# Performance work log

Measured on AMD Instinct MI355X. Metric: run time of the kernel, lower is better.

## Reference

```python
import jax, jax.numpy as jnp
import numpy as np

B, S, HID = 1, 2048, 2880
H, KV, D = 64, 8, 64
WINDOW = 128
SCALE = D ** -0.5
NEG_INF = jnp.float32(-1e30)


def _rope_cos_sin():
    # realistic RoPE tables over full head_dim (HF rotate_half convention)
    inv_freq = 1.0 / (10000.0 ** (np.arange(0, D, 2, dtype=np.float32) / D))
    t = np.arange(S, dtype=np.float32)
    freqs = np.outer(t, inv_freq)                      # [S, D/2]
    emb = np.concatenate([freqs, freqs], axis=-1)      # [S, D]
    return jnp.asarray(np.cos(emb))[None], jnp.asarray(np.sin(emb))[None]


def setup_inputs() -> dict:
    key = jax.random.key(0)
    ks = jax.random.split(key, 10)
    cos, sin = _rope_cos_sin()
    sd = lambda fan_in: 1.0 / np.sqrt(fan_in)
    return {
        "hidden_states": jax.random.normal(ks[0], (B, S, HID), jnp.float32),
        "cos": cos, "sin": sin,
        "Wq": jax.random.normal(ks[1], (HID, H * D), jnp.float32) * sd(HID),
        "bq": jax.random.normal(ks[2], (H * D,), jnp.float32) * 0.02,
        "Wk": jax.random.normal(ks[3], (HID, KV * D), jnp.float32) * sd(HID),
        "bk": jax.random.normal(ks[4], (KV * D,), jnp.float32) * 0.02,
        "Wv": jax.random.normal(ks[5], (HID, KV * D), jnp.float32) * sd(HID),
        "bv": jax.random.normal(ks[6], (KV * D,), jnp.float32) * 0.02,
        "Wo": jax.random.normal(ks[7], (H * D, HID), jnp.float32) * sd(H * D),
        "bo": jax.random.normal(ks[8], (HID,), jnp.float32) * 0.02,
        "sinks": jax.random.normal(ks[9], (H,), jnp.float32),
    }


def _rotate_half(x):
    x1, x2 = jnp.split(x, 2, axis=-1)
    return jnp.concatenate([-x2, x1], axis=-1)


def _forward(hidden_states, cos, sin, Wq, bq, Wk, bk, Wv, bv, Wo, bo, sinks):
    q = (hidden_states @ Wq + bq).reshape(B, S, H, D)
    k = (hidden_states @ Wk + bk).reshape(B, S, KV, D)
    v = (hidden_states @ Wv + bv).reshape(B, S, KV, D)
    # RoPE with explicit cos/sin, unsqueeze at head dim (bsnd layout)
    c, s = cos[:, :, None, :], sin[:, :, None, :]
    q = q * c + _rotate_half(q) * s
    k = k * c + _rotate_half(k) * s
    # GQA: expand kv heads to match query heads
    k = jnp.repeat(k, H // KV, axis=2)
    v = jnp.repeat(v, H // KV, axis=2)
    scores = jnp.einsum("bqhd,bkhd->bhqk", q, k) * SCALE  # [B,H,S,S]
    i = jnp.arange(S)[:, None]
    j = jnp.arange(S)[None, :]
    allowed = (j <= i) & (j > i - WINDOW)                  # causal + sliding window
    scores = jnp.where(allowed, scores, NEG_INF)
    # sink-augmented softmax: sinks act as an extra logit per head, dropped after norm
    m = jnp.maximum(scores.max(axis=-1), sinks[None, :, None])  # [B,H,S]
    p = jnp.exp(scores - m[..., None])                      # [B,H,S,S]
    denom = p.sum(axis=-1) + jnp.exp(sinks[None, :, None] - m)  # [B,H,S]
    attn = jnp.einsum("bhqk,bkhd->bqhd", p, v) / denom.transpose(0, 2, 1)[..., None]
    return attn.reshape(B, S, H * D) @ Wo + bo


def reference(hidden_states, cos, sin, Wq, bq, Wk, bk, Wv, bv, Wo, bo, sinks):
    return _forward(hidden_states, cos, sin, Wq, bq, Wk, bk, Wv, bv, Wo, bo, sinks)
```

## Files before the change

kernel.cpp:

```cpp
#include <hip/hip_runtime.h>

typedef unsigned short u16;
typedef __bf16 bf16x8 __attribute__((ext_vector_type(8)));
typedef float f32x4 __attribute__((ext_vector_type(4)));

constexpr int SEQ = 2048;
constexpr int HIDN = 2880;
constexpr int NQKV = 5120;
constexpr float SCALE = 0.125f;
constexpr float NEG_INF = -1e30f;

#define ASM_VMCNT(n)  asm volatile("s_waitcnt vmcnt(" #n ")" ::: "memory")
#define ASM_LGKM(n)   asm volatile("s_waitcnt lgkmcnt(" #n ")" ::: "memory")
#define ASM_BARRIER() asm volatile("s_barrier" ::: "memory")
#define SCHEDBAR()    __builtin_amdgcn_sched_barrier(0)

__device__ __forceinline__ u16 f2bf(float f) {
  unsigned int u = __builtin_bit_cast(unsigned int, f);
  u += 0x7FFFu + ((u >> 16) & 1u);
  return (u16)(u >> 16);
}
__device__ __forceinline__ float bf2f(u16 h) {
  unsigned int u = ((unsigned int)h) << 16;
  return __builtin_bit_cast(float, u);
}
__device__ __forceinline__ void async_load16(const void* g, void* l) {
  __builtin_amdgcn_global_load_lds(
      (const __attribute__((address_space(1))) unsigned int*)g,
      (__attribute__((address_space(3))) unsigned int*)l, 16, 0, 0);
}
__device__ __forceinline__ f32x4 DSR(unsigned addr) {
  f32x4 d;
  asm volatile("ds_read_b128 %0, %1" : "=v"(d) : "v"(addr));
  return d;
}
__device__ __forceinline__ bf16x8 asbf(f32x4 v) { return __builtin_bit_cast(bf16x8, v); }

__global__ __launch_bounds__(256) void conv_f2b(const float* __restrict__ in,
                                                u16* __restrict__ out, long n4) {
  long i = (long)blockIdx.x * 256 + threadIdx.x;
  if (i >= n4) return;
  float4 v = ((const float4*)in)[i];
  u16 o0 = f2bf(v.x), o1 = f2bf(v.y), o2 = f2bf(v.z), o3 = f2bf(v.w);
  out[i * 4 + 0] = o0; out[i * 4 + 1] = o1; out[i * 4 + 2] = o2; out[i * 4 + 3] = o3;
}

__global__ __launch_bounds__(256) void transpose_f2b(const float* __restrict__ in,
                                                     u16* __restrict__ out,
                                                     int R, int C, int ostride) {
  __shared__ float tile[32][33];
  int c0 = blockIdx.x * 32, r0 = blockIdx.y * 32;
  int tx = threadIdx.x & 31, ty = threadIdx.x >> 5;
#pragma unroll
  for (int i = 0; i < 32; i += 8)
    tile[ty + i][tx] = in[(long)(r0 + ty + i) * C + c0 + tx];
  __syncthreads();
#pragma unroll
  for (int i = 0; i < 32; i += 8)
    out[(long)(c0 + ty + i) * ostride + r0 + tx] = f2bf(tile[tx][ty + i]);
}

__global__ __launch_bounds__(256) void concat_bias(const float* bq, const float* bk,
                                                   const float* bv, float* out) {
  int t = blockIdx.x * 256 + threadIdx.x;
  if (t < 4096) out[t] = bq[t];
  else if (t < 4608) out[t] = bk[t - 4096];
  else if (t < 5120) out[t] = bv[t - 4608];
}

template <int MODE>
__global__ __launch_bounds__(256, 2) void gemm_p2(const u16* __restrict__ A,
                                                  const u16* __restrict__ Bp,
                                                  const float* __restrict__ bias,
                                                  const float* __restrict__ cosb,
                                                  const float* __restrict__ sinb,
                                                  void* __restrict__ out0,
                                                  float* __restrict__ out1,
                                                  int N, int Kst, int nkt) {
  __shared__ u16 lds[28672];
  const int tid = threadIdx.x, lane = tid & 63, wid = tid >> 6;
  const int lr = lane & 15, lk = lane >> 4;

  const int gm = gridDim.x;
  int nwg = gm * gridDim.y;
  int bid = blockIdx.y * gm + blockIdx.x;
  int q8 = nwg >> 3, r8 = nwg & 7;
  int xcd = bid & 7, seq = bid >> 3;
  int swz = (xcd < r8 ? xcd * (q8 + 1) : r8 * (q8 + 1) + (xcd - r8) * q8) + seq;
  const long brow = (long)(swz % gm) * 128;
  const long bcol = (long)(swz / gm) * 256;
  const long kbase = (MODE == 1) ? (long)blockIdx.z * nkt * 32 : 0;

  char* L = (char*)lds;
  const u16* Asrc[2];
  const u16* Bsrc[4];
#pragma unroll
  for (int i = 0; i < 2; ++i) {
    int c = tid + 256 * i;
    Asrc[i] = A + (brow + (c >> 2)) * (long)Kst + kbase + ((c & 3) ^ ((c >> 3) & 3)) * 8;
  }
#pragma unroll
  for (int i = 0; i < 4; ++i) {
    int c = tid + 256 * i;
    Bsrc[i] = Bp + (bcol + (c >> 2)) * (long)Kst + kbase + ((c & 3) ^ ((c >> 3) & 3)) * 8;
  }
  auto stageA = [&](int kt, int ab) {
    char* d = L + ab * 8192;
    async_load16(Asrc[0] + (long)kt * 32, d + tid * 16);
    async_load16(Asrc[1] + (long)kt * 32, d + (tid + 256) * 16);
  };
  auto stageB = [&](int kt) {
    char* d = L + 24576 + (kt & 1) * 16384;
#pragma unroll
    for (int i = 0; i < 4; ++i)
      async_load16(Bsrc[i] + (long)kt * 32, d + (tid + 256 * i) * 16);
  };

  const unsigned lds0 = (unsigned)(size_t)L;
  const unsigned xs = (unsigned)((lk ^ ((lr >> 1) & 3)) << 4);
  const unsigned aoff = lds0 + (unsigned)(lr * 64) + xs;
  const unsigned boff = lds0 + 24576u + (unsigned)((wid * 64 + lr) * 64) + xs;

  f32x4 acc[8][4] = {};
  stageA(0, 0); stageB(0); stageA(1, 1); stageB(1);
  ASM_VMCNT(6);
  ASM_BARRIER();

  int a3 = 0;
  for (int t = 0; t < nkt; ++t) {
    const unsigned ab = aoff + (unsigned)(a3 * 8192);
    const unsigned bb = boff + (unsigned)((t & 1) * 16384);
    const bool s2 = (t + 2 < nkt);
    const int a3n = (a3 == 2) ? 0 : a3 + 1;
    const int a3s = (a3n == 2) ? 0 : a3n + 1;
    f32x4 a[4], b[4];
#pragma unroll
    for (int mf = 0; mf < 4; ++mf) a[mf] = DSR(ab + mf * 1024u);
#pragma unroll
    for (int nf = 0; nf < 4; ++nf) b[nf] = DSR(bb + nf * 1024u);
    if (s2) stageA(t + 2, a3s);
    ASM_BARRIER();
    ASM_LGKM(0); SCHEDBAR();
    __builtin_amdgcn_s_setprio(1);
#pragma unroll
    for (int mf = 0; mf < 4; ++mf)
#pragma unroll
      for (int nf = 0; nf < 4; ++nf)
        acc[mf][nf] = __builtin_amdgcn_mfma_f32_16x16x32_bf16(asbf(a[mf]), asbf(b[nf]), acc[mf][nf], 0, 0, 0);
    __builtin_amdgcn_s_setprio(0);
    ASM_BARRIER();
#pragma unroll
    for (int mf = 0; mf < 4; ++mf) a[mf] = DSR(ab + (mf + 4) * 1024u);
    if (s2) stageB(t + 2);
    ASM_BARRIER();
    ASM_LGKM(0); SCHEDBAR();
    __builtin_amdgcn_s_setprio(1);
#pragma unroll
    for (int mf = 0; mf < 4; ++mf)
#pragma unroll
      for (int nf = 0; nf < 4; ++nf)
        acc[mf + 4][nf] = __builtin_amdgcn_mfma_f32_16x16x32_bf16(asbf(a[mf]), asbf(b[nf]), acc[mf + 4][nf], 0, 0, 0);
    __builtin_amdgcn_s_setprio(0);
    if (s2) { ASM_VMCNT(6); } else { ASM_VMCNT(0); }
    ASM_BARRIER();
    a3 = a3n;
  }

  const int col0 = (int)bcol + wid * 64;
  if (MODE == 0) {
    const bool rope = (col0 < 4608);
#pragma unroll
    for (int mf = 0; mf < 8; ++mf) {
      long row = brow + mf * 16 + lk * 4;
#pragma unroll
      for (int r = 0; r < 4; ++r) {
        long s = row + r;
        if (rope) {
#pragma unroll
          for (int nf = 0; nf < 2; ++nf) {
            int col = col0 + nf * 16 + lr;
            int d = nf * 16 + lr;
            float c = cosb[s * 64 + d], sn = sinb[s * 64 + d];
            float x1 = acc[mf][nf][r] + bias[col];
            float x2 = acc[mf][nf + 2][r] + bias[col + 32];
            ((u16*)out0)[s * (long)N + col]      = f2bf(x1 * c - x2 * sn);
            ((u16*)out0)[s * (long)N + col + 32] = f2bf(x2 * c + x1 * sn);
          }
        } else {
#pragma unroll
          for (int nf = 0; nf < 4; ++nf) {
            int col = col0 + nf * 16 + lr;
            ((u16*)out0)[s * (long)N + col] = f2bf(acc[mf][nf][r] + bias[col]);
          }
        }
      }
    }
  } else {
    float* o = (blockIdx.z == 0) ? (float*)out0 : out1;
#pragma unroll
    for (int mf = 0; mf < 8; ++mf) {
      long row = brow + mf * 16 + lk * 4;
#pragma unroll
      for (int nf = 0; nf < 4; ++nf) {
        int col = col0 + nf * 16 + lr;
        if (col < N) {
#pragma unroll
          for (int r = 0; r < 4; ++r)
            o[(row + r) * (long)N + col] = acc[mf][nf][r];
        }
      }
    }
  }
}

__global__ __launch_bounds__(256) void combine_out(const float* __restrict__ P1,
                                                   const float* __restrict__ bias,
                                                   float* __restrict__ out) {
  long i = (long)blockIdx.x * 256 + threadIdx.x;
  if (i >= (long)SEQ * HIDN / 4) return;
  int c4 = (int)(i % (HIDN / 4));
  float4 p0 = ((const float4*)out)[i];
  float4 p1 = ((const float4*)P1)[i];
  float4 b = ((const float4*)bias)[c4];
  float4 r;
  r.x = p0.x + p1.x + b.x; r.y = p0.y + p1.y + b.y;
  r.z = p0.z + p1.z + b.z; r.w = p0.w + p1.w + b.w;
  ((float4*)out)[i] = r;
}

__global__ __launch_bounds__(256, 1) void attn_kernel(const u16* __restrict__ QKV,
                                                      const float* __restrict__ sinks,
                                                      u16* __restrict__ Oa) {
  __shared__ u16 Ks[64 * 64];
  __shared__ u16 Vt[64 * 64];
  __shared__ u16 Ps[4][64 * 72];
  const int tid = threadIdx.x, wid = tid >> 6, lane = tid & 63;
  const int lr = lane & 15, lk = lane >> 4;
  const int i0 = blockIdx.x * 64;
  const int h = blockIdx.y * 4 + wid;
  const int g = h >> 3;

  bf16x8 qf[4][2];
#pragma unroll
  for (int m = 0; m < 4; ++m)
#pragma unroll
    for (int kc = 0; kc < 2; ++kc)
      qf[m][kc] = *(const bf16x8*)&QKV[(long)(i0 + m * 16 + lr) * NQKV + h * 64 + kc * 32 + lk * 8];

  const float sinkh = sinks[h];
  float mrun[4][4], lrun[4][4];
  f32x4 oacc[4][4] = {};
#pragma unroll
  for (int m = 0; m < 4; ++m)
#pragma unroll
    for (int r = 0; r < 4; ++r) { mrun[m][r] = sinkh; lrun[m][r] = 0.f; }

  const int jb0 = (i0 >= 128) ? (i0 - 128) : 0;
  for (int jb = jb0; jb <= i0; jb += 64) {
#pragma unroll
    for (int i = 0; i < 2; ++i) {
      int c = wid * 128 + i * 64 + lane;
      int row = c >> 3, sp = c & 7;
      int ssrc = sp ^ (row & 7);
      async_load16(QKV + (long)(jb + row) * NQKV + 4096 + g * 64 + ssrc * 8,
                   ((char*)Ks) + c * 16);
    }
    {
      int j0 = (tid & 31) * 2, d0 = (tid >> 5) * 8;
      const u16* vp = QKV + (long)(jb + j0) * NQKV + 4608 + g * 64 + d0;
      int4 rv0 = *(const int4*)vp;
      int4 rv1 = *(const int4*)(vp + NQKV);
      const u16* a0 = (const u16*)&rv0;
      const u16* a1 = (const u16*)&rv1;
#pragma unroll
      for (int e = 0; e < 8; ++e) {
        int d = d0 + e;
        unsigned val = (unsigned)a0[e] | ((unsigned)a1[e] << 16);
        int byt = d * 128 + ((((j0 >> 3) ^ (d & 7)) << 4)) + ((j0 & 7) * 2);
        *(unsigned*)((char*)Vt + byt) = val;
      }
    }
    __syncthreads();

    f32x4 sf[4][4] = {};
    __builtin_amdgcn_s_setprio(1);
#pragma unroll
    for (int kc = 0; kc < 2; ++kc) {
      bf16x8 kf[4];
#pragma unroll
      for (int cf = 0; cf < 4; ++cf) {
        int row = cf * 16 + lr;
        kf[cf] = *(const bf16x8*)((const char*)Ks + row * 128 + (((kc * 4 + lk) ^ (lr & 7)) << 4));
      }
#pragma unroll
      for (int m = 0; m < 4; ++m)
#pragma unroll
        for (int cf = 0; cf < 4; ++cf)
          sf[m][cf] = __builtin_amdgcn_mfma_f32_16x16x32_bf16(qf[m][kc], kf[cf], sf[m][cf], 0, 0, 0);
    }
    __builtin_amdgcn_s_setprio(0);

#pragma unroll
    for (int m = 0; m < 4; ++m) {
      float rmax[4];
#pragma unroll
      for (int r = 0; r < 4; ++r) {
        int i = i0 + m * 16 + lk * 4 + r;
        float mx = NEG_INF;
#pragma unroll
        for (int cf = 0; cf < 4; ++cf) {
          int j = jb + cf * 16 + lr;
          float v = sf[m][cf][r] * SCALE;
          bool ok = (j <= i) && (j > i - 128);
          v = ok ? v : NEG_INF;
          sf[m][cf][r] = v;
          mx = fmaxf(mx, v);
        }
#pragma unroll
        for (int off = 1; off < 16; off <<= 1) mx = fmaxf(mx, __shfl_xor(mx, off, 64));
        rmax[r] = mx;
      }
#pragma unroll
      for (int r = 0; r < 4; ++r) {
        float mnew = fmaxf(mrun[m][r], rmax[r]);
        float corr = __expf(mrun[m][r] - mnew);
        mrun[m][r] = mnew;
        float rsum = 0.f;
#pragma unroll
        for (int cf = 0; cf < 4; ++cf) {
          float p = __expf(sf[m][cf][r] - mnew);
          sf[m][cf][r] = p;
          rsum += p;
        }
#pragma unroll
        for (int off = 1; off < 16; off <<= 1) rsum += __shfl_xor(rsum, off, 64);
        lrun[m][r] = lrun[m][r] * corr + rsum;
#pragma unroll
        for (int dn = 0; dn < 4; ++dn) oacc[m][dn][r] *= corr;
      }
    }

#pragma unroll
    for (int m = 0; m < 4; ++m)
#pragma unroll
      for (int cf = 0; cf < 4; ++cf)
#pragma unroll
        for (int r = 0; r < 4; ++r)
          Ps[wid][(m * 16 + lk * 4 + r) * 72 + cf * 16 + lr] = f2bf(sf[m][cf][r]);
    __syncthreads();

    __builtin_amdgcn_s_setprio(1);
#pragma unroll
    for (int kc = 0; kc < 2; ++kc) {
      bf16x8 pf[4], vf[4];
#pragma unroll
      for (int m = 0; m < 4; ++m)
        pf[m] = *(const bf16x8*)&Ps[wid][(m * 16 + lr) * 72 + kc * 32 + lk * 8];
#pragma unroll
      for (int dn = 0; dn < 4; ++dn) {
        int row = dn * 16 + lr;
        vf[dn] = *(const bf16x8*)((const char*)Vt + row * 128 + (((kc * 4 + lk) ^ (lr & 7)) << 4));
      }
#pragma unroll
      for (int m = 0; m < 4; ++m)
#pragma unroll
        for (int dn = 0; dn < 4; ++dn)
          oacc[m][dn] = __builtin_amdgcn_mfma_f32_16x16x32_bf16(pf[m], vf[dn], oacc[m][dn], 0, 0, 0);
    }
    __builtin_amdgcn_s_setprio(0);
    __syncthreads();
  }

#pragma unroll
  for (int m = 0; m < 4; ++m)
#pragma unroll
    for (int r = 0; r < 4; ++r) {
      float denom = lrun[m][r] + __expf(sinkh - mrun[m][r]);
      float inv = 1.f / denom;
      long row = i0 + m * 16 + lk * 4 + r;
#pragma unroll
      for (int dn = 0; dn < 4; ++dn)
        Oa[row * 4096 + h * 64 + dn * 16 + lr] = f2bf(oacc[m][dn][r] * inv);
    }
}

extern "C" void kernel_launch(void* const* d_in, const int* in_sizes, int n_in,
                              void* d_out, int out_size, void* d_ws, size_t ws_size,
                              hipStream_t stream) {
  const float* X    = (const float*)d_in[0];
  const float* cosb = (const float*)d_in[1];
  const float* sinb = (const float*)d_in[2];
  const float* Wq   = (const float*)d_in[3];
  const float* bq   = (const float*)d_in[4];
  const float* Wk   = (const float*)d_in[5];
  const float* bk   = (const float*)d_in[6];
  const float* Wv   = (const float*)d_in[7];
  const float* bv   = (const float*)d_in[8];
  const float* Wo   = (const float*)d_in[9];
  const float* bo   = (const float*)d_in[10];
  const float* sinks = (const float*)d_in[11];

  char* ws = (char*)d_ws;
  size_t off = 0;
  auto alloc = [&](size_t bytes) -> void* {
    void* p = ws + off;
    off += (bytes + 255) & ~(size_t)255;
    return p;
  };
  u16*   Xb    = (u16*)alloc((size_t)SEQ * HIDN * 2);
  u16*   Wqkv  = (u16*)alloc((size_t)NQKV * HIDN * 2);
  u16*   Wot   = (u16*)alloc((size_t)3072 * 4096 * 2);
  float* bqkv  = (float*)alloc((size_t)NQKV * 4);
  u16*   QKV   = (u16*)alloc((size_t)SEQ * NQKV * 2);
  u16*   Ab    = (u16*)alloc((size_t)SEQ * 4096 * 2);
  float* Pt1 = (float*)Wqkv;
  (void)ws_size; (void)in_sizes; (void)n_in; (void)out_size;

  conv_f2b<<<(SEQ * HIDN / 4 + 255) / 256, 256, 0, stream>>>(X, Xb, (long)SEQ * HIDN / 4);
  transpose_f2b<<<dim3(4096 / 32, HIDN / 32), 256, 0, stream>>>(Wq, Wqkv, HIDN, 4096, HIDN);
  transpose_f2b<<<dim3(512 / 32, HIDN / 32), 256, 0, stream>>>(Wk, Wqkv + (size_t)4096 * HIDN, HIDN, 512, HIDN);
  transpose_f2b<<<dim3(512 / 32, HIDN / 32), 256, 0, stream>>>(Wv, Wqkv + (size_t)4608 * HIDN, HIDN, 512, HIDN);
  transpose_f2b<<<dim3(HIDN / 32, 4096 / 32), 256, 0, stream>>>(Wo, Wot, 4096, HIDN, 4096);
  concat_bias<<<(NQKV + 255) / 256, 256, 0, stream>>>(bq, bk, bv, bqkv);
  gemm_p2<0><<<dim3(16, 20, 1), 256, 0, stream>>>(Xb, Wqkv, bqkv, cosb, sinb,
                                                  QKV, nullptr, NQKV, HIDN, 90);
  attn_kernel<<<dim3(SEQ / 64, 64 / 4), 256, 0, stream>>>(QKV, sinks, Ab);
  gemm_p2<1><<<dim3(16, 12, 2), 256, 0, stream>>>(Ab, Wot, nullptr, nullptr, nullptr,
                                                  d_out, Pt1, HIDN, 4096, 64);
  combine_out<<<(SEQ * HIDN / 4 + 255) / 256, 256, 0, stream>>>(Pt1, bo, (float*)d_out);
}
```

Baseline: 246.8 us.

## Use 8-wave 256x256 GEMM tiles and merge QKV weight transposes into one launch

Result: no change. 246.3 us (-0.2%).

```diff
diff --git a/kernel.cpp b/kernel.cpp
--- a/kernel.cpp
+++ b/kernel.cpp
@@ -45,6 +45,26 @@
   out[i * 4 + 0] = o0; out[i * 4 + 1] = o1; out[i * 4 + 2] = o2; out[i * 4 + 3] = o3;
 }
 
+__global__ __launch_bounds__(256) void transpose_qkv(const float* __restrict__ Wq,
+                                                     const float* __restrict__ Wk,
+                                                     const float* __restrict__ Wv,
+                                                     u16* __restrict__ out) {
+  __shared__ float tile[32][33];
+  int c0 = blockIdx.x * 32, r0 = blockIdx.y * 32;
+  int tx = threadIdx.x & 31, ty = threadIdx.x >> 5;
+  const float* src; int C, cl;
+  if (c0 < 4096)      { src = Wq; C = 4096; cl = c0; }
+  else if (c0 < 4608) { src = Wk; C = 512;  cl = c0 - 4096; }
+  else                { src = Wv; C = 512;  cl = c0 - 4608; }
+#pragma unroll
+  for (int i = 0; i < 32; i += 8)
+    tile[ty + i][tx] = src[(long)(r0 + ty + i) * C + cl + tx];
+  __syncthreads();
+#pragma unroll
+  for (int i = 0; i < 32; i += 8)
+    out[(long)(c0 + ty + i) * HIDN + r0 + tx] = f2bf(tile[tx][ty + i]);
+}
+
 __global__ __launch_bounds__(256) void transpose_f2b(const float* __restrict__ in,
                                                      u16* __restrict__ out,
                                                      int R, int C, int ostride) {
@@ -69,7 +89,7 @@
 }
 
 template <int MODE>
-__global__ __launch_bounds__(256, 2) void gemm_p2(const u16* __restrict__ A,
+__global__ __launch_bounds__(512, 2) void gemm_8w(const u16* __restrict__ A,
                                                   const u16* __restrict__ Bp,
                                                   const float* __restrict__ bias,
                                                   const float* __restrict__ cosb,
@@ -77,8 +97,9 @@
                                                   void* __restrict__ out0,
                                                   float* __restrict__ out1,
                                                   int N, int Kst, int nkt) {
-  __shared__ u16 lds[28672];
+  __shared__ u16 lds[40960];
   const int tid = threadIdx.x, lane = tid & 63, wid = tid >> 6;
+  const int wm = wid >> 2, wn = wid & 3;
   const int lr = lane & 15, lk = lane >> 4;
 
   const int gm = gridDim.x;
@@ -87,48 +108,44 @@
   int q8 = nwg >> 3, r8 = nwg & 7;
   int xcd = bid & 7, seq = bid >> 3;
   int swz = (xcd < r8 ? xcd * (q8 + 1) : r8 * (q8 + 1) + (xcd - r8) * q8) + seq;
-  const long brow = (long)(swz % gm) * 128;
+  const long brow = (long)(swz % gm) * 256;
   const long bcol = (long)(swz / gm) * 256;
   const long kbase = (MODE == 1) ? (long)blockIdx.z * nkt * 32 : 0;
 
   char* L = (char*)lds;
   const u16* Asrc[2];
-  const u16* Bsrc[4];
+  const u16* Bsrc[2];
 #pragma unroll
   for (int i = 0; i < 2; ++i) {
-    int c = tid + 256 * i;
-    Asrc[i] = A + (brow + (c >> 2)) * (long)Kst + kbase + ((c & 3) ^ ((c >> 3) & 3)) * 8;
-  }
-#pragma unroll
-  for (int i = 0; i < 4; ++i) {
-    int c = tid + 256 * i;
-    Bsrc[i] = Bp + (bcol + (c >> 2)) * (long)Kst + kbase + ((c & 3) ^ ((c >> 3) & 3)) * 8;
+    int c = tid + 512 * i;
+    long ks = kbase + ((c & 3) ^ ((c >> 3) & 3)) * 8;
+    Asrc[i] = A  + (brow + (c >> 2)) * (long)Kst + ks;
+    Bsrc[i] = Bp + (bcol + (c >> 2)) * (long)Kst + ks;
   }
   auto stageA = [&](int kt, int ab) {
-    char* d = L + ab * 8192;
+    char* d = L + ab * 16384;
     async_load16(Asrc[0] + (long)kt * 32, d + tid * 16);
-    async_load16(Asrc[1] + (long)kt * 32, d + (tid + 256) * 16);
+    async_load16(Asrc[1] + (long)kt * 32, d + (tid + 512) * 16);
   };
-  auto stageB = [&](int kt) {
-    char* d = L + 24576 + (kt & 1) * 16384;
-#pragma unroll
-    for (int i = 0; i < 4; ++i)
-      async_load16(Bsrc[i] + (long)kt * 32, d + (tid + 256 * i) * 16);
+  auto stageB = [&](int kt, int bb) {
+    char* d = L + 49152 + bb * 16384;
+    async_load16(Bsrc[0] + (long)kt * 32, d + tid * 16);
+    async_load16(Bsrc[1] + (long)kt * 32, d + (tid + 512) * 16);
   };
 
   const unsigned lds0 = (unsigned)(size_t)L;
   const unsigned xs = (unsigned)((lk ^ ((lr >> 1) & 3)) << 4);
-  const unsigned aoff = lds0 + (unsigned)(lr * 64) + xs;
-  const unsigned boff = lds0 + 24576u + (unsigned)((wid * 64 + lr) * 64) + xs;
+  const unsigned aoff = lds0 + (unsigned)((wm * 128 + lr) * 64) + xs;
+  const unsigned boff = lds0 + 49152u + (unsigned)((wn * 64 + lr) * 64) + xs;
 
   f32x4 acc[8][4] = {};
-  stageA(0, 0); stageB(0); stageA(1, 1); stageB(1);
-  ASM_VMCNT(6);
+  stageA(0, 0); stageB(0, 0); stageA(1, 1); stageB(1, 1);
+  ASM_VMCNT(4);
   ASM_BARRIER();
 
   int a3 = 0;
   for (int t = 0; t < nkt; ++t) {
-    const unsigned ab = aoff + (unsigned)(a3 * 8192);
+    const unsigned ab = aoff + (unsigned)(a3 * 16384);
     const unsigned bb = boff + (unsigned)((t & 1) * 16384);
     const bool s2 = (t + 2 < nkt);
     const int a3n = (a3 == 2) ? 0 : a3 + 1;
@@ -151,7 +168,7 @@
     ASM_BARRIER();
 #pragma unroll
     for (int mf = 0; mf < 4; ++mf) a[mf] = DSR(ab + (mf + 4) * 1024u);
-    if (s2) stageB(t + 2);
+    if (s2) stageB(t + 2, t & 1);
     ASM_BARRIER();
     ASM_LGKM(0); SCHEDBAR();
     __builtin_amdgcn_s_setprio(1);
@@ -161,17 +178,17 @@
       for (int nf = 0; nf < 4; ++nf)
         acc[mf + 4][nf] = __builtin_amdgcn_mfma_f32_16x16x32_bf16(asbf(a[mf]), asbf(b[nf]), acc[mf + 4][nf], 0, 0, 0);
     __builtin_amdgcn_s_setprio(0);
-    if (s2) { ASM_VMCNT(6); } else { ASM_VMCNT(0); }
+    if (s2) { ASM_VMCNT(4); } else { ASM_VMCNT(0); }
     ASM_BARRIER();
     a3 = a3n;
   }
 
-  const int col0 = (int)bcol + wid * 64;
+  const int col0 = (int)bcol + wn * 64;
   if (MODE == 0) {
     const bool rope = (col0 < 4608);
 #pragma unroll
     for (int mf = 0; mf < 8; ++mf) {
-      long row = brow + mf * 16 + lk * 4;
+      long row = brow + wm * 128 + mf * 16 + lk * 4;
 #pragma unroll
       for (int r = 0; r < 4; ++r) {
         long s = row + r;
@@ -199,7 +216,7 @@
     float* o = (blockIdx.z == 0) ? (float*)out0 : out1;
 #pragma unroll
     for (int mf = 0; mf < 8; ++mf) {
-      long row = brow + mf * 16 + lk * 4;
+      long row = brow + wm * 128 + mf * 16 + lk * 4;
 #pragma unroll
       for (int nf = 0; nf < 4; ++nf) {
         int col = col0 + nf * 16 + lr;
@@ -417,15 +434,13 @@
   (void)ws_size; (void)in_sizes; (void)n_in; (void)out_size;
 
   conv_f2b<<<(SEQ * HIDN / 4 + 255) / 256, 256, 0, stream>>>(X, Xb, (long)SEQ * HIDN / 4);
-  transpose_f2b<<<dim3(4096 / 32, HIDN / 32), 256, 0, stream>>>(Wq, Wqkv, HIDN, 4096, HIDN);
-  transpose_f2b<<<dim3(512 / 32, HIDN / 32), 256, 0, stream>>>(Wk, Wqkv + (size_t)4096 * HIDN, HIDN, 512, HIDN);
-  transpose_f2b<<<dim3(512 / 32, HIDN / 32), 256, 0, stream>>>(Wv, Wqkv + (size_t)4608 * HIDN, HIDN, 512, HIDN);
+  transpose_qkv<<<dim3(NQKV / 32, HIDN / 32), 256, 0, stream>>>(Wq, Wk, Wv, Wqkv);
   transpose_f2b<<<dim3(HIDN / 32, 4096 / 32), 256, 0, stream>>>(Wo, Wot, 4096, HIDN, 4096);
   concat_bias<<<(NQKV + 255) / 256, 256, 0, stream>>>(bq, bk, bv, bqkv);
-  gemm_p2<0><<<dim3(16, 20, 1), 256, 0, stream>>>(Xb, Wqkv, bqkv, cosb, sinb,
-                                                  QKV, nullptr, NQKV, HIDN, 90);
+  gemm_8w<0><<<dim3(8, 20, 1), 512, 0, stream>>>(Xb, Wqkv, bqkv, cosb, sinb,
+                                                 QKV, nullptr, NQKV, HIDN, 90);
   attn_kernel<<<dim3(SEQ / 64, 64 / 4), 256, 0, stream>>>(QKV, sinks, Ab);
-  gemm_p2<1><<<dim3(16, 12, 2), 256, 0, stream>>>(Ab, Wot, nullptr, nullptr, nullptr,
-                                                  d_out, Pt1, HIDN, 4096, 64);
+  gemm_8w<1><<<dim3(8, 12, 2), 512, 0, stream>>>(Ab, Wot, nullptr, nullptr, nullptr,
+                                                 d_out, Pt1, HIDN, 4096, 64);
   combine_out<<<(SEQ * HIDN / 4 + 255) / 256, 256, 0, stream>>>(Pt1, bo, (float*)d_out);
 }
```
